# Kernel tuning notes

Hardware: AMD Instinct MI355X
Metric: run time of the kernel (lower is better)

## Reference

```python
import jax, jax.numpy as jnp
import numpy as np

B, F, C, O, M = 128, 4096, 32, 32, 9  # batch, num_fields, in_ch, out_ch, num_coeffs (moves incl. self)


def setup_inputs() -> dict:
    key = jax.random.key(0)
    k1, k2, k3, k4 = jax.random.split(key, 4)
    x = jax.random.normal(k1, (B, F, C), dtype=jnp.float32)
    # mask[m, f] = index of the source field feeding target field f via move m
    mask = jax.random.randint(k2, (M, F), 0, F, dtype=jnp.int32)
    init_std = 1.0 / (3.0 * np.sqrt(C * O))  # matches TruncatedNormal stddev in build()
    conv_coeffs = jax.random.normal(k3, (M, C, O), dtype=jnp.float32) * init_std
    # biases are zero-initialized in the original; use small random values so the
    # bias-add path is exercised numerically
    biases = jax.random.normal(k4, (F, O), dtype=jnp.float32) * 0.01
    return {"x": x, "mask": mask, "conv_coeffs": conv_coeffs, "biases": biases}


def reference(x, mask, conv_coeffs, biases):
    # ch_convolve_by_moves: gather source fields per move, per-move matmul, per-field bias.
    # gathered[b, m, f, c] = x[b, mask[m, f], c]
    gathered = jnp.take(x, mask, axis=1)              # [B, M, F, C]
    out = jnp.einsum('bmfc,mco->bfo', gathered, conv_coeffs)  # sum over moves and in-channels
    return out + biases                               # per-field bias broadcast over batch
```

## Files before the change

kernel.cpp:

```cpp
#include <hip/hip_runtime.h>


#define B_ 128
#define F_ 4096
#define C_ 32
#define O_ 32
#define M_ 9
#define T_ 18

typedef _Float16 halfx4 __attribute__((ext_vector_type(4)));
typedef _Float16 halfx8 __attribute__((ext_vector_type(8)));
typedef float floatx4 __attribute__((ext_vector_type(4)));
typedef float floatx16 __attribute__((ext_vector_type(16)));

__global__ __launch_bounds__(256) void pass1_cvt(
    const float* __restrict__ x, _Float16* __restrict__ xh)
{
    const int blk = blockIdx.x;
    const int xcd = blk & 7;
    const int ft  = (blk >> 3) & 127;
    const int p   = blk >> 10;
    const int b0  = (p * 8 + xcd) * 4;
    const int f0  = ft * 32;
    const int fl  = threadIdx.x >> 3;
    const int c4  = (threadIdx.x & 7) * 4;
    const int k   = c4 >> 4;
    const int h   = (c4 >> 3) & 1;
    const int j0  = c4 & 7;
    _Float16* dst = xh + (size_t)(f0 + fl) * (B_ * C_) + (b0 >> 2) * 128
                    + (k * 8 + h * 4) * 8 + j0;
#pragma unroll
    for (int q = 0; q < 4; ++q) {
        const floatx4 v = __builtin_nontemporal_load(
            reinterpret_cast<const floatx4*>(
                x + ((size_t)(b0 + q) * F_ + f0 + fl) * C_ + c4));
        halfx4 hv;
#pragma unroll
        for (int jj = 0; jj < 4; ++jj) hv[jj] = (_Float16)v[jj];
        *reinterpret_cast<halfx4*>(dst + q * 8) = hv;
    }
}

__global__ __launch_bounds__(256, 3) void pass2_gemm(
    const _Float16* __restrict__ xh, const int* __restrict__ mask,
    const float* __restrict__ coeffs, const float* __restrict__ biases,
    float* __restrict__ out)
{
    __shared__ _Float16 sw[T_ * 64 * 8];
    const int tid = threadIdx.x;

    for (int id = tid; id < T_ * 64; id += 256) {
        const int t  = id >> 6;
        const int L  = id & 63;
        const int m  = t >> 1;
        const int cb = 16 * (t & 1) + 8 * (L >> 5);
        const int oo = L & 31;
        halfx8 w;
#pragma unroll
        for (int jj = 0; jj < 8; ++jj)
            w[jj] = (_Float16)coeffs[(m * C_ + cb + jj) * O_ + oo];
        *reinterpret_cast<halfx8*>(&sw[id * 8]) = w;
    }
    __syncthreads();

    const int blk = blockIdx.x;
    const int xcd = blk & 7;
    const int ft  = (blk >> 3) & 127;
    const int p   = 3 - (blk >> 10);
    const int b0  = (p * 8 + xcd) * 4;
    const int f0  = ft * 32;

    const int wave = tid >> 6;
    const int lane = tid & 63;
    const int h    = lane >> 5;
    const int row  = lane & 31;
    const int fi   = row >> 2;
    const int bp   = row & 3;
    const int o    = lane & 31;
    const int fw   = f0 + wave * 8;
    const int f    = fw + fi;

    int sidx[M_];
#pragma unroll
    for (int m = 0; m < M_; ++m) sidx[m] = mask[m * F_ + f];

    const _Float16* xb = xh + (b0 >> 2) * 128 + (h * 4 + bp) * 8;

    halfx8 a[T_];
#pragma unroll
    for (int m = 0; m < M_; ++m) {
        const _Float16* rp = xb + (size_t)sidx[m] * (B_ * C_);
        a[2 * m]     = *reinterpret_cast<const halfx8*>(rp);
        a[2 * m + 1] = *reinterpret_cast<const halfx8*>(rp + 64);
    }

    floatx16 acc;
#pragma unroll
    for (int i = 0; i < 16; ++i) acc[i] = 0.0f;
#pragma unroll
    for (int t = 0; t < T_; ++t) {
        const halfx8 bwt = *reinterpret_cast<const halfx8*>(&sw[(t * 64 + lane) * 8]);
        acc = __builtin_amdgcn_mfma_f32_32x32x16_f16(a[t], bwt, acc, 0, 0, 0);
    }

    float bv[4];
#pragma unroll
    for (int q = 0; q < 4; ++q)
        bv[q] = biases[(size_t)(fw + 2 * q + h) * O_ + o];

#pragma unroll
    for (int r = 0; r < 16; ++r) {
        const int q   = r >> 2;
        const int obp = r & 3;
        const float v = acc[r] + bv[q];
        __builtin_nontemporal_store(
            v, &out[((size_t)(b0 + obp) * F_ + fw + 2 * q + h) * O_ + o]);
    }
}

__global__ __launch_bounds__(256) void fallback_kernel(
    const float* __restrict__ x, const int* __restrict__ mask,
    const float* __restrict__ coeffs, const float* __restrict__ biases,
    float* __restrict__ out)
{
    int gid = blockIdx.x * 256 + threadIdx.x;
    int o = gid & (O_ - 1);
    int f = (gid >> 5) & (F_ - 1);
    int b = gid >> 17;
    float acc = biases[f * O_ + o];
    for (int m = 0; m < M_; ++m) {
        int s = mask[m * F_ + f];
        const float* xr = x + ((size_t)b * F_ + s) * C_;
        const float* wr = coeffs + (m * C_) * O_ + o;
#pragma unroll
        for (int c = 0; c < C_; ++c)
            acc += xr[c] * wr[c * O_];
    }
    out[gid] = acc;
}

extern "C" void kernel_launch(void* const* d_in, const int* in_sizes, int n_in,
                              void* d_out, int out_size, void* d_ws, size_t ws_size,
                              hipStream_t stream) {
    const float* x      = (const float*)d_in[0];
    const int*   mask   = (const int*)d_in[1];
    const float* coeffs = (const float*)d_in[2];
    const float* biases = (const float*)d_in[3];
    float* out = (float*)d_out;

    const size_t need = (size_t)F_ * B_ * C_ * sizeof(_Float16);
    if (ws_size >= need) {
        _Float16* xh = (_Float16*)d_ws;
        pass1_cvt<<<4 * 8 * 128, 256, 0, stream>>>(x, xh);
        pass2_gemm<<<4 * 8 * 128, 256, 0, stream>>>(xh, mask, coeffs, biases, out);
    } else {
        fallback_kernel<<<(B_ * F_ * O_) / 256, 256, 0, stream>>>(x, mask, coeffs, biases, out);
    }
}
```

Before: 145.8 us.

## Replace static block mapping with XCD-aware atomic work queue and stealing

The gemm pass becomes a persistent-style kernel. Each workgroup reads its hardware XCC id and pulls chunks of two field tiles from a per-XCD atomic queue, so chunks that share batch rows stay on one die's L2. When that queue is empty it steals from a global queue, and a done-flag exchange ensures each chunk runs only once. This adds a memset launch, several atomics and barriers per chunk, and relies on the undocumented s_getreg encoding.

```diff
diff --git a/kernel.cpp b/kernel.cpp
--- a/kernel.cpp
+++ b/kernel.cpp
@@ -7,6 +7,8 @@
 #define O_ 32
 #define M_ 9
 #define T_ 18
+#define CHUNKS_PER_XCD 256
+#define CHUNKS_TOTAL 2048
 
 typedef _Float16 halfx4 __attribute__((ext_vector_type(4)));
 typedef _Float16 halfx8 __attribute__((ext_vector_type(8)));
@@ -41,12 +43,60 @@
     }
 }
 
+__device__ __forceinline__ void process_tile(
+    const _Float16* __restrict__ xh, const int* __restrict__ mask,
+    const float* __restrict__ biases, float* __restrict__ out,
+    const _Float16* sw, int b0, int f0,
+    int wave, int lane, int h, int fi, int bp, int o)
+{
+    const int fw = f0 + wave * 8;
+    const int f  = fw + fi;
+
+    int sidx[M_];
+#pragma unroll
+    for (int m = 0; m < M_; ++m) sidx[m] = mask[m * F_ + f];
+
+    const _Float16* xb = xh + (b0 >> 2) * 128 + (h * 4 + bp) * 8;
+
+    halfx8 a[T_];
+#pragma unroll
+    for (int m = 0; m < M_; ++m) {
+        const _Float16* rp = xb + (size_t)sidx[m] * (B_ * C_);
+        a[2 * m]     = *reinterpret_cast<const halfx8*>(rp);
+        a[2 * m + 1] = *reinterpret_cast<const halfx8*>(rp + 64);
+    }
+
+    floatx16 acc;
+#pragma unroll
+    for (int i = 0; i < 16; ++i) acc[i] = 0.0f;
+#pragma unroll
+    for (int t = 0; t < T_; ++t) {
+        const halfx8 bwt = *reinterpret_cast<const halfx8*>(&sw[(t * 64 + lane) * 8]);
+        acc = __builtin_amdgcn_mfma_f32_32x32x16_f16(a[t], bwt, acc, 0, 0, 0);
+    }
+
+    float bv[4];
+#pragma unroll
+    for (int q = 0; q < 4; ++q)
+        bv[q] = biases[(size_t)(fw + 2 * q + h) * O_ + o];
+
+#pragma unroll
+    for (int r = 0; r < 16; ++r) {
+        const int q   = r >> 2;
+        const int obp = r & 3;
+        const float v = acc[r] + bv[q];
+        __builtin_nontemporal_store(
+            v, &out[((size_t)(b0 + obp) * F_ + fw + 2 * q + h) * O_ + o]);
+    }
+}
+
 __global__ __launch_bounds__(256, 3) void pass2_gemm(
     const _Float16* __restrict__ xh, const int* __restrict__ mask,
     const float* __restrict__ coeffs, const float* __restrict__ biases,
-    float* __restrict__ out)
+    float* __restrict__ out, int* __restrict__ qctr, int* __restrict__ done)
 {
     __shared__ _Float16 sw[T_ * 64 * 8];
+    __shared__ int s_msg;
     const int tid = threadIdx.x;
 
     for (int id = tid; id < T_ * 64; id += 256) {
@@ -61,14 +111,6 @@
             w[jj] = (_Float16)coeffs[(m * C_ + cb + jj) * O_ + oo];
         *reinterpret_cast<halfx8*>(&sw[id * 8]) = w;
     }
-    __syncthreads();
-
-    const int blk = blockIdx.x;
-    const int xcd = blk & 7;
-    const int ft  = (blk >> 3) & 127;
-    const int p   = 3 - (blk >> 10);
-    const int b0  = (p * 8 + xcd) * 4;
-    const int f0  = ft * 32;
 
     const int wave = tid >> 6;
     const int lane = tid & 63;
@@ -77,44 +119,49 @@
     const int fi   = row >> 2;
     const int bp   = row & 3;
     const int o    = lane & 31;
-    const int fw   = f0 + wave * 8;
-    const int f    = fw + fi;
-
-    int sidx[M_];
-#pragma unroll
-    for (int m = 0; m < M_; ++m) sidx[m] = mask[m * F_ + f];
-
-    const _Float16* xb = xh + (b0 >> 2) * 128 + (h * 4 + bp) * 8;
-
-    halfx8 a[T_];
-#pragma unroll
-    for (int m = 0; m < M_; ++m) {
-        const _Float16* rp = xb + (size_t)sidx[m] * (B_ * C_);
-        a[2 * m]     = *reinterpret_cast<const halfx8*>(rp);
-        a[2 * m + 1] = *reinterpret_cast<const halfx8*>(rp + 64);
-    }
-
-    floatx16 acc;
-#pragma unroll
-    for (int i = 0; i < 16; ++i) acc[i] = 0.0f;
-#pragma unroll
-    for (int t = 0; t < T_; ++t) {
-        const halfx8 bwt = *reinterpret_cast<const halfx8*>(&sw[(t * 64 + lane) * 8]);
-        acc = __builtin_amdgcn_mfma_f32_32x32x16_f16(a[t], bwt, acc, 0, 0, 0);
-    }
-
-    float bv[4];
-#pragma unroll
-    for (int q = 0; q < 4; ++q)
-        bv[q] = biases[(size_t)(fw + 2 * q + h) * O_ + o];
-
-#pragma unroll
-    for (int r = 0; r < 16; ++r) {
-        const int q   = r >> 2;
-        const int obp = r & 3;
-        const float v = acc[r] + bv[q];
-        __builtin_nontemporal_store(
-            v, &out[((size_t)(b0 + obp) * F_ + fw + 2 * q + h) * O_ + o]);
+
+    int xcc;
+    asm volatile("s_getreg_b32 %0, 0xf814" : "=s"(xcc));
+    xcc &= 7;
+
+    for (;;) {
+        __syncthreads();
+        if (tid == 0) s_msg = atomicAdd(&qctr[xcc], 1);
+        __syncthreads();
+        const int c = s_msg;
+        if (c >= CHUNKS_PER_XCD) break;
+        __syncthreads();
+        if (tid == 0) s_msg = atomicExch(&done[xcc * CHUNKS_PER_XCD + c], 1);
+        __syncthreads();
+        if (s_msg) continue;
+        const int phase = c >> 6;
+        const int ft0   = (c & 63) * 2;
+        const int b0    = (phase * 8 + xcc) * 4;
+        process_tile(xh, mask, biases, out, sw, b0, ft0 * 32,
+                     wave, lane, h, fi, bp, o);
+        process_tile(xh, mask, biases, out, sw, b0, (ft0 + 1) * 32,
+                     wave, lane, h, fi, bp, o);
+    }
+
+    for (;;) {
+        __syncthreads();
+        if (tid == 0) s_msg = atomicAdd(&qctr[8], 1);
+        __syncthreads();
+        const int g = s_msg;
+        if (g >= CHUNKS_TOTAL) break;
+        __syncthreads();
+        if (tid == 0) s_msg = atomicExch(&done[g], 1);
+        __syncthreads();
+        if (s_msg) continue;
+        const int xv    = g >> 8;
+        const int c     = g & (CHUNKS_PER_XCD - 1);
+        const int phase = c >> 6;
+        const int ft0   = (c & 63) * 2;
+        const int b0    = (phase * 8 + xv) * 4;
+        process_tile(xh, mask, biases, out, sw, b0, ft0 * 32,
+                     wave, lane, h, fi, bp, o);
+        process_tile(xh, mask, biases, out, sw, b0, (ft0 + 1) * 32,
+                     wave, lane, h, fi, bp, o);
     }
 }
 
@@ -148,12 +195,17 @@
     const float* biases = (const float*)d_in[3];
     float* out = (float*)d_out;
 
-    const size_t need = (size_t)F_ * B_ * C_ * sizeof(_Float16);
-    if (ws_size >= need) {
+    const size_t xh_bytes  = (size_t)F_ * B_ * C_ * sizeof(_Float16);
+    const size_t ctl_bytes = (16 + CHUNKS_TOTAL) * sizeof(int);
+    if (ws_size >= xh_bytes + ctl_bytes) {
         _Float16* xh = (_Float16*)d_ws;
-        pass1_cvt<<<4 * 8 * 128, 256, 0, stream>>>(x, xh);
-        pass2_gemm<<<4 * 8 * 128, 256, 0, stream>>>(xh, mask, coeffs, biases, out);
+        int* ctl = (int*)((char*)d_ws + xh_bytes);
+        hipMemsetAsync(ctl, 0, ctl_bytes, stream);
+        pass1_cvt<<<4096, 256, 0, stream>>>(x, xh);
+        pass2_gemm<<<CHUNKS_TOTAL, 256, 0, stream>>>(
+            xh, mask, coeffs, biases, out, ctl, ctl + 16);
     } else {
-        fallback_kernel<<<(B_ * F_ * O_) / 256, 256, 0, stream>>>(x, mask, coeffs, biases, out);
-    }
-}
+        fallback_kernel<<<(B_ * F_ * O_) / 256, 256, 0, stream>>>(
+            x, mask, coeffs, biases, out);
+    }
+}
```

Result: slower. 221.7 us (+52.1%).
